# Optimization experiments

Measured on AMD Instinct MI355X. Metric: run time of the kernel, lower is better.

## Reference

```python
import jax, jax.numpy as jnp
import numpy as np

N = 100000
E = 1600000
D_IN = 128
HID = 128
OUT = 64


def _sage_conv(x, edge_index, W_l, W_r, b, num_nodes):
    # PyG SAGEConv (aggr='mean'): out = lin_l(mean_{j in N(i)} x_j) + lin_r(x_i)
    src, dst = edge_index[0], edge_index[1]
    msgs = x[src]  # [E, d] gather from source nodes
    summed = jax.ops.segment_sum(msgs, dst, num_segments=num_nodes)  # [N, d]
    cnt = jax.ops.segment_sum(jnp.ones((msgs.shape[0],), x.dtype), dst, num_segments=num_nodes)
    agg = summed / jnp.maximum(cnt, 1.0)[:, None]  # mean; isolated nodes -> 0
    return agg @ W_l + b + x @ W_r


def setup_inputs() -> dict:
    key = jax.random.key(0)
    ks = jax.random.split(key, 8)
    x = jax.random.normal(ks[0], (N, D_IN), dtype=jnp.float32)
    edge_index = jax.random.randint(ks[1], (2, E), 0, N, dtype=jnp.int64)
    s1 = 1.0 / np.sqrt(D_IN)
    s2 = 1.0 / np.sqrt(HID)
    W_l1 = jax.random.uniform(ks[2], (D_IN, HID), jnp.float32, -s1, s1)
    W_r1 = jax.random.uniform(ks[3], (D_IN, HID), jnp.float32, -s1, s1)
    b1 = jnp.zeros((HID,), jnp.float32)
    W_l2 = jax.random.uniform(ks[4], (HID, OUT), jnp.float32, -s2, s2)
    W_r2 = jax.random.uniform(ks[5], (HID, OUT), jnp.float32, -s2, s2)
    b2 = jnp.zeros((OUT,), jnp.float32)
    return {"x": x, "edge_index": edge_index, "W_l1": W_l1, "W_r1": W_r1,
            "b1": b1, "W_l2": W_l2, "W_r2": W_r2, "b2": b2}


def reference(x, edge_index, W_l1, W_r1, b1, W_l2, W_r2, b2):
    h = _sage_conv(x, edge_index, W_l1, W_r1, b1, N)
    h = jax.nn.relu(h)
    out = _sage_conv(h, edge_index, W_l2, W_r2, b2, N)
    return out
```

## Files before the change

kernel.cpp:

```cpp
#include <hip/hip_runtime.h>
#include <hip/hip_fp16.h>

typedef __attribute__((ext_vector_type(8))) short bf16x8;
typedef __attribute__((ext_vector_type(4))) float f32x4;

__device__ __forceinline__ f32x4 mfma16(bf16x8 a, bf16x8 b, f32x4 c) {
    return __builtin_amdgcn_mfma_f32_16x16x32_bf16(a, b, c, 0, 0, 0);
}

__device__ __forceinline__ unsigned short bf16_rte(float f) {
    unsigned int u = __float_as_uint(f);
    unsigned int r = (u + 0x7FFFu + ((u >> 16) & 1u)) >> 16;
    return (unsigned short)r;
}
__device__ __forceinline__ float bf16_f(unsigned short h) {
    return __uint_as_float(((unsigned int)h) << 16);
}

__device__ __forceinline__ void split8h(bf16x8 raw, bf16x8& hi, bf16x8& lo) {
#pragma unroll
    for (int j = 0; j < 8; ++j) {
        float f = __half2float(__ushort_as_half((unsigned short)raw[j]));
        unsigned short h = bf16_rte(f);
        hi[j] = (short)h;
        lo[j] = (short)bf16_rte(f - bf16_f(h));
    }
}

__device__ __forceinline__ void acc8(uint4 r, float4& A0, float4& A1) {
    float2 v0 = __half22float2(*(const __half2*)&r.x);
    float2 v1 = __half22float2(*(const __half2*)&r.y);
    float2 v2 = __half22float2(*(const __half2*)&r.z);
    float2 v3 = __half22float2(*(const __half2*)&r.w);
    A0.x += v0.x; A0.y += v0.y; A0.z += v1.x; A0.w += v1.y;
    A1.x += v2.x; A1.y += v2.y; A1.z += v3.x; A1.w += v3.y;
}

__device__ __forceinline__ void acc4(uint2 r, float4& A) {
    float2 v0 = __half22float2(*(const __half2*)&r.x);
    float2 v1 = __half22float2(*(const __half2*)&r.y);
    A.x += v0.x; A.y += v0.y; A.z += v1.x; A.w += v1.y;
}

#define MAXNB 1024

__global__ __launch_bounds__(256) void k_prep(
    const float* __restrict__ Wl1, const float* __restrict__ Wr1,
    const float* __restrict__ Wl2, const float* __restrict__ Wr2,
    unsigned short* __restrict__ w1ah, unsigned short* __restrict__ w1al,
    unsigned short* __restrict__ w1bh, unsigned short* __restrict__ w1bl,
    unsigned short* __restrict__ w2ah, unsigned short* __restrict__ w2al,
    unsigned short* __restrict__ w2bh, unsigned short* __restrict__ w2bl,
    const float* __restrict__ x, unsigned short* __restrict__ x16,
    const int* __restrict__ dst, int* __restrict__ bcnt,
    int E, int chunk, int xb, int nb, int total8) {
    __shared__ int hh[MAXNB];
    int b = blockIdx.x;
    int t = threadIdx.x;
    if (b < 192) {
        const float* W;
        unsigned short *hi, *lo;
        int F, e;
        if (b < 64)       { W = Wl1; hi = w1ah; lo = w1al; F = 128; e = b * 256 + t; }
        else if (b < 128) { W = Wr1; hi = w1bh; lo = w1bl; F = 128; e = (b - 64) * 256 + t; }
        else if (b < 160) { W = Wl2; hi = w2ah; lo = w2al; F = 64;  e = (b - 128) * 256 + t; }
        else              { W = Wr2; hi = w2bh; lo = w2bl; F = 64;  e = (b - 160) * 256 + t; }
        if (e >= 128 * F) return;
        int col = e >> 7, k = e & 127;
        float v = W[(size_t)k * F + col];
        unsigned short h = bf16_rte(v);
        hi[e] = h;
        lo[e] = bf16_rte(v - bf16_f(h));
    } else if (b < 192 + xb) {
        int i = (b - 192) * 256 + t;
        if (i >= total8) return;
        const float4* xp = (const float4*)x + (size_t)i * 2;
        float4 a = xp[0], bb = xp[1];
        bf16x8 o;
        o[0] = (short)__half_as_ushort(__float2half_rn(a.x));
        o[1] = (short)__half_as_ushort(__float2half_rn(a.y));
        o[2] = (short)__half_as_ushort(__float2half_rn(a.z));
        o[3] = (short)__half_as_ushort(__float2half_rn(a.w));
        o[4] = (short)__half_as_ushort(__float2half_rn(bb.x));
        o[5] = (short)__half_as_ushort(__float2half_rn(bb.y));
        o[6] = (short)__half_as_ushort(__float2half_rn(bb.z));
        o[7] = (short)__half_as_ushort(__float2half_rn(bb.w));
        *(bf16x8*)&x16[(size_t)i * 8] = o;
    } else {
        int cb = b - 192 - xb;
        for (int i = t; i < nb; i += 256) hh[i] = 0;
        __syncthreads();
        int base = cb * chunk;
        int end = min(base + chunk, E);
        for (int i = base + t; i < end; i += 256) atomicAdd(&hh[dst[i] >> 7], 1);
        __syncthreads();
        for (int i = t; i < nb; i += 256)
            if (hh[i]) atomicAdd(&bcnt[i], hh[i]);
    }
}


__global__ void k_bscan(const int* __restrict__ bcnt, int* __restrict__ boff,
                        int* __restrict__ bcur, int nb) {
    __shared__ int sh[1024];
    int t = threadIdx.x;
    int v = (t < nb) ? bcnt[t] : 0;
    sh[t] = v;
    __syncthreads();
    for (int off = 1; off < 1024; off <<= 1) {
        int u = (t >= off) ? sh[t - off] : 0;
        __syncthreads();
        sh[t] += u;
        __syncthreads();
    }
    if (t < nb) {
        int ex = sh[t] - v;
        boff[t] = ex;
        bcur[t] = ex;
    }
}

__global__ __launch_bounds__(256) void k_bscatter(
    const int* __restrict__ src, const int* __restrict__ dst,
    int* __restrict__ bcur, unsigned int* __restrict__ pairs,
    int E, int chunk, int nb) {
    __shared__ int h[MAXNB];
    __shared__ int curs[MAXNB];
    int t = threadIdx.x;
    for (int i = t; i < nb; i += 256) h[i] = 0;
    __syncthreads();
    int base = blockIdx.x * chunk;
    int end = min(base + chunk, E);
    for (int i = base + t; i < end; i += 256) atomicAdd(&h[dst[i] >> 7], 1);
    __syncthreads();
    for (int i = t; i < nb; i += 256)
        curs[i] = h[i] ? atomicAdd(&bcur[i], h[i]) : 0;
    __syncthreads();
    for (int i = base + t; i < end; i += 256) {
        int d = dst[i];
        int p = atomicAdd(&curs[d >> 7], 1);
        pairs[p] = ((unsigned int)(d & 127) << 25) | (unsigned int)src[i];
    }
}

__global__ __launch_bounds__(256) void k_build(
    const unsigned int* __restrict__ pairs, const int* __restrict__ boff,
    int* __restrict__ csr, int* __restrict__ start, int* __restrict__ deg,
    int n, int nb, int E) {
    __shared__ int scnt[128];
    __shared__ int soff[128];
    __shared__ int cur[128];
    int b = blockIdx.x;
    int t = threadIdx.x;
    int base = boff[b];
    int end = (b + 1 < nb) ? boff[b + 1] : E;
    if (t < 128) scnt[t] = 0;
    __syncthreads();
    for (int i = base + t; i < end; i += 256) {
        unsigned int e = pairs[i];
        atomicAdd(&scnt[e >> 25], 1);
    }
    __syncthreads();
    if (t < 128) soff[t] = scnt[t];
    __syncthreads();
    for (int off = 1; off < 128; off <<= 1) {
        int val = 0;
        if (t < 128 && t >= off) val = soff[t - off];
        __syncthreads();
        if (t < 128) soff[t] += val;
        __syncthreads();
    }
    if (t < 128) {
        int c = scnt[t];
        int ex = soff[t] - c;
        int node = b * 128 + t;
        if (node < n) {
            start[node] = base + ex;
            deg[node] = c;
        }
        cur[t] = base + ex;
    }
    __syncthreads();
    for (int i = base + t; i < end; i += 256) {
        unsigned int e = pairs[i];
        int p = atomicAdd(&cur[e >> 25], 1);
        csr[p] = (int)(e & 0x1FFFFFFu);
    }
}

#define SR 40

__global__ __launch_bounds__(256) void aggF(
    const unsigned short* __restrict__ tab, const int* __restrict__ csr,
    const int* __restrict__ start, const int* __restrict__ deg,
    unsigned short* __restrict__ outm, int n) {
    int gid = blockIdx.x * blockDim.x + threadIdx.x;
    int wave = gid >> 6, lane = gid & 63;
    int sub = lane >> 4, fl = lane & 15;
    int node = wave * 4 + sub;
    if (node >= n) return;
    int s = start[node], d = deg[node];
    float4 A0 = {0.f, 0.f, 0.f, 0.f}, A1 = {0.f, 0.f, 0.f, 0.f};
    int j = 0;
    if (d >= 4) {
        int i0 = csr[s], i1 = csr[s + 1], i2 = csr[s + 2], i3 = csr[s + 3];
        for (; j + 8 <= d; j += 4) {
            int n0 = csr[s + j + 4], n1 = csr[s + j + 5];
            int n2 = csr[s + j + 6], n3 = csr[s + j + 7];
            uint4 r0 = ((const uint4*)(tab + (size_t)i0 * 128))[fl];
            uint4 r1 = ((const uint4*)(tab + (size_t)i1 * 128))[fl];
            uint4 r2 = ((const uint4*)(tab + (size_t)i2 * 128))[fl];
            uint4 r3 = ((const uint4*)(tab + (size_t)i3 * 128))[fl];
            acc8(r0, A0, A1); acc8(r1, A0, A1);
            acc8(r2, A0, A1); acc8(r3, A0, A1);
            i0 = n0; i1 = n1; i2 = n2; i3 = n3;
        }
        {
            uint4 r0 = ((const uint4*)(tab + (size_t)i0 * 128))[fl];
            uint4 r1 = ((const uint4*)(tab + (size_t)i1 * 128))[fl];
            uint4 r2 = ((const uint4*)(tab + (size_t)i2 * 128))[fl];
            uint4 r3 = ((const uint4*)(tab + (size_t)i3 * 128))[fl];
            acc8(r0, A0, A1); acc8(r1, A0, A1);
            acc8(r2, A0, A1); acc8(r3, A0, A1);
            j += 4;
        }
    }
    for (; j < d; ++j)
        acc8(((const uint4*)(tab + (size_t)csr[s + j] * 128))[fl], A0, A1);
    float inv = 1.0f / (float)max(d, 1);
    __half2 h0 = __floats2half2_rn(A0.x * inv, A0.y * inv);
    __half2 h1 = __floats2half2_rn(A0.z * inv, A0.w * inv);
    __half2 h2 = __floats2half2_rn(A1.x * inv, A1.y * inv);
    __half2 h3 = __floats2half2_rn(A1.z * inv, A1.w * inv);
    uint4 w;
    w.x = *(unsigned int*)&h0;
    w.y = *(unsigned int*)&h1;
    w.z = *(unsigned int*)&h2;
    w.w = *(unsigned int*)&h3;
    *(uint4*)&outm[(size_t)node * 128 + fl * 8] = w;
}

__global__ __launch_bounds__(256, 4) void fused12(
    const unsigned short* __restrict__ X, const unsigned short* __restrict__ XM,
    const unsigned short* __restrict__ W0H, const unsigned short* __restrict__ W0L,
    const unsigned short* __restrict__ W1H, const unsigned short* __restrict__ W1L,
    const float* __restrict__ b1,
    const unsigned short* __restrict__ W2aH, const unsigned short* __restrict__ W2aL,
    const unsigned short* __restrict__ W2bH, const unsigned short* __restrict__ W2bL,
    const float* __restrict__ b2,
    unsigned short* __restrict__ p16, float* __restrict__ outF, int n) {
    constexpr int CT = 2;
    __shared__ unsigned short lds[4 * 64 * SR];
    unsigned short* hi0 = lds;
    unsigned short* hi1 = lds + 64 * SR;
    unsigned short* lo0 = lds + 2 * 64 * SR;
    unsigned short* lo1 = lds + 3 * 64 * SR;

    int t = threadIdx.x;
    int wv = t >> 6, l = t & 63, q = l >> 4, nl = l & 15;
    int node0 = blockIdx.x * 64;
    int sn = t >> 2, q4 = t & 3;
    int gn = min(node0 + sn, n - 1);
    int sbase = sn * SR + q4 * 8;

    bf16x8 xr[4], s1r[4];
    {
        const unsigned short* p = X + (size_t)gn * 128 + q4 * 8;
#pragma unroll
        for (int c = 0; c < 4; ++c) xr[c] = *(const bf16x8*)(p + c * 32);
        const unsigned short* pm = XM + (size_t)gn * 128 + q4 * 8;
#pragma unroll
        for (int c = 0; c < 4; ++c) s1r[c] = *(const bf16x8*)(pm + c * 32);
    }

    f32x4 acc[4][CT];
#pragma unroll
    for (int a = 0; a < 4; ++a)
#pragma unroll
        for (int b = 0; b < CT; ++b) acc[a][b] = (f32x4){0.f, 0.f, 0.f, 0.f};

    bf16x8 whA[CT], wlA[CT], whB[CT], wlB[CT];
    int wcX = wv * 32;

#define LOAD_W(AH, AL, WHp, WLp, CC)                                       \
    {                                                                      \
        _Pragma("unroll") for (int uu = 0; uu < CT; ++uu) {                \
            int wb = (wcX + uu * 16 + nl) * 128 + (CC) * 32 + q * 8;       \
            AH[uu] = *(const bf16x8*)&(WHp)[wb];                           \
            AL[uu] = *(const bf16x8*)&(WLp)[wb];                           \
        }                                                                  \
    }

#define STAGE_CHUNK(HP, LP, RAW)                                           \
    {                                                                      \
        bf16x8 _hi, _lo;                                                   \
        split8h(RAW, _hi, _lo);                                            \
        *(bf16x8*)&(HP)[sbase] = _hi;                                      \
        *(bf16x8*)&(LP)[sbase] = _lo;                                      \
    }

#define MFMA_CHUNK(HP, LP, WHR, WLR)                                       \
    {                                                                      \
        bf16x8 ah[4], al[4];                                               \
        _Pragma("unroll") for (int tt = 0; tt < 4; ++tt) {                 \
            int off = (tt * 16 + nl) * SR + q * 8;                         \
            ah[tt] = *(const bf16x8*)&(HP)[off];                           \
            al[tt] = *(const bf16x8*)&(LP)[off];                           \
        }                                                                  \
        _Pragma("unroll") for (int tt = 0; tt < 4; ++tt)                   \
            _Pragma("unroll") for (int uu = 0; uu < CT; ++uu) {            \
                f32x4 a = acc[tt][uu];                                     \
                a = mfma16(al[tt], WHR[uu], a);                            \
                a = mfma16(ah[tt], WLR[uu], a);                            \
                a = mfma16(ah[tt], WHR[uu], a);                            \
                acc[tt][uu] = a;                                           \
            }                                                              \
    }

#define PHASE(RSRC, WHp, WLp)                                              \
    LOAD_W(whA, wlA, WHp, WLp, 0);                                         \
    STAGE_CHUNK(hi0, lo0, RSRC[0]);                                        \
    __syncthreads();                                                       \
    LOAD_W(whB, wlB, WHp, WLp, 1);                                         \
    STAGE_CHUNK(hi1, lo1, RSRC[1]);                                        \
    MFMA_CHUNK(hi0, lo0, whA, wlA);                                        \
    __syncthreads();                                                       \
    LOAD_W(whA, wlA, WHp, WLp, 2);                                         \
    STAGE_CHUNK(hi0, lo0, RSRC[2]);                                        \
    MFMA_CHUNK(hi1, lo1, whB, wlB);                                        \
    __syncthreads();                                                       \
    LOAD_W(whB, wlB, WHp, WLp, 3);                                         \
    STAGE_CHUNK(hi1, lo1, RSRC[3]);                                        \
    MFMA_CHUNK(hi0, lo0, whA, wlA);                                        \
    __syncthreads();                                                       \
    MFMA_CHUNK(hi1, lo1, whB, wlB);                                        \
    __syncthreads();

    PHASE(xr, W0H, W0L);
    PHASE(s1r, W1H, W1L);

    unsigned short* tb = lds;
#pragma unroll
    for (int uu = 0; uu < CT; ++uu) {
        int col = wcX + uu * 16 + nl;
        float bv = b1[col];
#pragma unroll
        for (int tt = 0; tt < 4; ++tt)
#pragma unroll
            for (int r = 0; r < 4; ++r) {
                float vv = fmaxf(acc[tt][uu][r] + bv, 0.f);
                tb[(tt * 16 + q * 4 + r) * 136 + col] =
                    __half_as_ushort(__float2half_rn(vv));
            }
    }
    __syncthreads();
    bf16x8 hreg[4];
    {
        const unsigned short* sp = tb + sn * 136 + q4 * 8;
#pragma unroll
        for (int c = 0; c < 4; ++c) hreg[c] = *(const bf16x8*)(sp + c * 32);
    }
    __syncthreads();

#pragma unroll
    for (int a = 0; a < 4; ++a)
#pragma unroll
        for (int b = 0; b < CT; ++b) acc[a][b] = (f32x4){0.f, 0.f, 0.f, 0.f};
    int ysel = wv >> 1;
    wcX = (wv & 1) * 32;
    const unsigned short* W2H = ysel ? W2bH : W2aH;
    const unsigned short* W2L = ysel ? W2bL : W2aL;
    PHASE(hreg, W2H, W2L);

#undef PHASE
#undef MFMA_CHUNK
#undef STAGE_CHUNK
#undef LOAD_W

    if (ysel) {
#pragma unroll
        for (int uu = 0; uu < CT; ++uu) {
            int col = wcX + uu * 16 + nl;
            float bv = b2[col];
#pragma unroll
            for (int tt = 0; tt < 4; ++tt)
#pragma unroll
                for (int r = 0; r < 4; ++r) {
                    int node = node0 + tt * 16 + q * 4 + r;
                    if (node < n) outF[(size_t)node * 64 + col] = acc[tt][uu][r] + bv;
                }
        }
    } else {
        unsigned short* tbu = lds;
#pragma unroll
        for (int uu = 0; uu < CT; ++uu) {
            int col = wcX + uu * 16 + nl;
#pragma unroll
            for (int tt = 0; tt < 4; ++tt)
#pragma unroll
                for (int r = 0; r < 4; ++r)
                    tbu[(tt * 16 + q * 4 + r) * 72 + col] =
                        __half_as_ushort(__float2half_rn(acc[tt][uu][r]));
        }
    }
    __syncthreads();
    {
        int node = node0 + sn;
        if (node < n) {
            const unsigned short* spu = lds + sn * 72 + q4 * 16;
            unsigned short* dpu = p16 + (size_t)node * 64 + q4 * 16;
            *(bf16x8*)dpu = *(const bf16x8*)spu;
            *(bf16x8*)(dpu + 8) = *(const bf16x8*)(spu + 8);
        }
    }
}

__global__ __launch_bounds__(256) void aggP(
    const unsigned short* __restrict__ tab, const int* __restrict__ csr,
    const int* __restrict__ start, const int* __restrict__ deg,
    float* __restrict__ outF, int n) {
    int gid = blockIdx.x * blockDim.x + threadIdx.x;
    int wave = gid >> 6, lane = gid & 63;
    int sub = lane >> 4, fl = lane & 15;
    int node = wave * 4 + sub;
    if (node >= n) return;
    int s = start[node], d = deg[node];
    float4 A = {0.f, 0.f, 0.f, 0.f};
    int j = 0;
    if (d >= 8) {
        int idx[8];
#pragma unroll
        for (int k = 0; k < 8; ++k) idx[k] = csr[s + k];
        for (; j + 16 <= d; j += 8) {
            uint2 rr[8];
#pragma unroll
            for (int k = 0; k < 8; ++k)
                rr[k] = ((const uint2*)(tab + (size_t)idx[k] * 64))[fl];
#pragma unroll
            for (int k = 0; k < 8; ++k) idx[k] = csr[s + j + 8 + k];
#pragma unroll
            for (int k = 0; k < 8; ++k) acc4(rr[k], A);
        }
        {
            uint2 rr[8];
#pragma unroll
            for (int k = 0; k < 8; ++k)
                rr[k] = ((const uint2*)(tab + (size_t)idx[k] * 64))[fl];
#pragma unroll
            for (int k = 0; k < 8; ++k) acc4(rr[k], A);
            j += 8;
        }
    }
    for (; j < d; ++j)
        acc4(((const uint2*)(tab + (size_t)csr[s + j] * 64))[fl], A);
    float inv = 1.0f / (float)max(d, 1);
    float* op = outF + (size_t)node * 64 + fl * 4;
    float4 cur = *(float4*)op;
    cur.x += A.x * inv;
    cur.y += A.y * inv;
    cur.z += A.z * inv;
    cur.w += A.w * inv;
    *(float4*)op = cur;
}


extern "C" void kernel_launch(void* const* d_in, const int* in_sizes, int n_in,
                              void* d_out, int out_size, void* d_ws, size_t ws_size,
                              hipStream_t stream) {
    const float* x   = (const float*)d_in[0];
    const int*   ei  = (const int*)d_in[1];
    const float* Wl1 = (const float*)d_in[2];
    const float* Wr1 = (const float*)d_in[3];
    const float* b1  = (const float*)d_in[4];
    const float* Wl2 = (const float*)d_in[5];
    const float* Wr2 = (const float*)d_in[6];
    const float* b2  = (const float*)d_in[7];
    float* out = (float*)d_out;

    int Nn = in_sizes[0] / 128;
    int E  = in_sizes[1] / 2;
    const int* src = ei;
    const int* dst = ei + E;
    int nb = (Nn + 127) / 128;

    char* ws = (char*)d_ws;
    auto alloc = [&](size_t bytes) -> char* {
        char* pp = ws;
        ws += (bytes + 255) / 256 * 256;
        return pp;
    };
    int* bcnt   = (int*)alloc((size_t)nb * 4);
    int* boff   = (int*)alloc((size_t)nb * 4);
    int* bcur   = (int*)alloc((size_t)nb * 4);
    int* start  = (int*)alloc((size_t)Nn * 4);
    int* deg    = (int*)alloc((size_t)Nn * 4);
    int* csr    = (int*)alloc((size_t)E * 4);
    unsigned short* x16  = (unsigned short*)alloc((size_t)Nn * 128 * 2);
    unsigned short* xm16 = (unsigned short*)alloc((size_t)Nn * 128 * 2);
    unsigned short* p16  = (unsigned short*)alloc((size_t)Nn * 64 * 2);
    unsigned short* w1ah = (unsigned short*)alloc(128 * 128 * 2);
    unsigned short* w1al = (unsigned short*)alloc(128 * 128 * 2);
    unsigned short* w1bh = (unsigned short*)alloc(128 * 128 * 2);
    unsigned short* w1bl = (unsigned short*)alloc(128 * 128 * 2);
    unsigned short* w2ah = (unsigned short*)alloc(64 * 128 * 2);
    unsigned short* w2al = (unsigned short*)alloc(64 * 128 * 2);
    unsigned short* w2bh = (unsigned short*)alloc(64 * 128 * 2);
    unsigned short* w2bl = (unsigned short*)alloc(64 * 128 * 2);
    unsigned int* pairs = (unsigned int*)p16;

    hipMemsetAsync(bcnt, 0, (size_t)nb * 4, stream);

    int total8 = Nn * 16;
    int xb = (total8 + 255) / 256;
    int nchunks = 256;
    int chunk = (E + nchunks - 1) / nchunks;
    k_prep<<<192 + xb + nchunks, 256, 0, stream>>>(
        Wl1, Wr1, Wl2, Wr2,
        w1ah, w1al, w1bh, w1bl, w2ah, w2al, w2bh, w2bl,
        x, x16, dst, bcnt, E, chunk, xb, nb, total8);

    k_bscan<<<1, 1024, 0, stream>>>(bcnt, boff, bcur, nb);
    k_bscatter<<<nchunks, 256, 0, stream>>>(src, dst, bcur, pairs, E, chunk, nb);
    k_build<<<nb, 256, 0, stream>>>(pairs, boff, csr, start, deg, Nn, nb, E);

    int gb = (Nn + 63) / 64;
    int ga = (Nn + 15) / 16;
    aggF<<<ga, 256, 0, stream>>>(x16, csr, start, deg, xm16, Nn);
    fused12<<<gb, 256, 0, stream>>>(x16, xm16,
                                    w1bh, w1bl, w1ah, w1al, b1,
                                    w2ah, w2al, w2bh, w2bl, b2,
                                    p16, out, Nn);
    aggP<<<ga, 256, 0, stream>>>(p16, csr, start, deg, out, Nn);
}
```

Before: 329.2 us.

## Build CSR with per-node global atomics instead of two-level bucket sort

Replaces the bucketed counting sort (block-level LDS histograms, pair scatter into buckets, then per-bucket local sort) with per-node degree counting via global atomics, a two-level scan for node offsets, and a direct atomic scatter of sources into CSR. This removes the intermediate packed-pairs pass and the k_build kernel, reducing edge-array traffic. In exchange it relies on millions of global atomics to scattered addresses and adds extra small launches; neighbor order within a row becomes nondeterministic.

```diff
diff --git a/kernel.cpp b/kernel.cpp
--- a/kernel.cpp
+++ b/kernel.cpp
@@ -52,9 +52,8 @@
     unsigned short* __restrict__ w2ah, unsigned short* __restrict__ w2al,
     unsigned short* __restrict__ w2bh, unsigned short* __restrict__ w2bl,
     const float* __restrict__ x, unsigned short* __restrict__ x16,
-    const int* __restrict__ dst, int* __restrict__ bcnt,
-    int E, int chunk, int xb, int nb, int total8) {
-    __shared__ int hh[MAXNB];
+    const int* __restrict__ dst, int* __restrict__ deg,
+    int E, int chunk, int xb, int total8) {
     int b = blockIdx.x;
     int t = threadIdx.x;
     if (b < 192) {
@@ -88,20 +87,30 @@
         *(bf16x8*)&x16[(size_t)i * 8] = o;
     } else {
         int cb = b - 192 - xb;
-        for (int i = t; i < nb; i += 256) hh[i] = 0;
-        __syncthreads();
         int base = cb * chunk;
         int end = min(base + chunk, E);
-        for (int i = base + t; i < end; i += 256) atomicAdd(&hh[dst[i] >> 7], 1);
+        for (int i = base + t; i < end; i += 256)
+            atomicAdd(&deg[dst[i]], 1);
+    }
+}
+
+
+__global__ __launch_bounds__(128) void k_bsum(
+    const int* __restrict__ deg, int* __restrict__ bcnt, int n) {
+    __shared__ int sh[128];
+    int b = blockIdx.x, t = threadIdx.x;
+    int node = b * 128 + t;
+    sh[t] = (node < n) ? deg[node] : 0;
+    __syncthreads();
+    for (int off = 64; off > 0; off >>= 1) {
+        if (t < off) sh[t] += sh[t + off];
         __syncthreads();
-        for (int i = t; i < nb; i += 256)
-            if (hh[i]) atomicAdd(&bcnt[i], hh[i]);
-    }
-}
-
+    }
+    if (t == 0) bcnt[b] = sh[0];
+}
 
 __global__ void k_bscan(const int* __restrict__ bcnt, int* __restrict__ boff,
-                        int* __restrict__ bcur, int nb) {
+                        int nb) {
     __shared__ int sh[1024];
     int t = threadIdx.x;
     int v = (t < nb) ? bcnt[t] : 0;
@@ -113,78 +122,41 @@
         sh[t] += u;
         __syncthreads();
     }
-    if (t < nb) {
-        int ex = sh[t] - v;
-        boff[t] = ex;
-        bcur[t] = ex;
-    }
-}
-
-__global__ __launch_bounds__(256) void k_bscatter(
+    if (t < nb) boff[t] = sh[t] - v;
+}
+
+__global__ __launch_bounds__(128) void k_nscan(
+    const int* __restrict__ deg, const int* __restrict__ boff,
+    int* __restrict__ start, int* __restrict__ cur, int n) {
+    __shared__ int sh[128];
+    int b = blockIdx.x, t = threadIdx.x;
+    int node = b * 128 + t;
+    int v = (node < n) ? deg[node] : 0;
+    sh[t] = v;
+    __syncthreads();
+    for (int off = 1; off < 128; off <<= 1) {
+        int u = (t >= off) ? sh[t - off] : 0;
+        __syncthreads();
+        sh[t] += u;
+        __syncthreads();
+    }
+    if (node < n) {
+        int ex = sh[t] - v + boff[b];
+        start[node] = ex;
+        cur[node] = ex;
+    }
+}
+
+__global__ __launch_bounds__(256) void k_scatter(
     const int* __restrict__ src, const int* __restrict__ dst,
-    int* __restrict__ bcur, unsigned int* __restrict__ pairs,
-    int E, int chunk, int nb) {
-    __shared__ int h[MAXNB];
-    __shared__ int curs[MAXNB];
-    int t = threadIdx.x;
-    for (int i = t; i < nb; i += 256) h[i] = 0;
-    __syncthreads();
-    int base = blockIdx.x * chunk;
-    int end = min(base + chunk, E);
-    for (int i = base + t; i < end; i += 256) atomicAdd(&h[dst[i] >> 7], 1);
-    __syncthreads();
-    for (int i = t; i < nb; i += 256)
-        curs[i] = h[i] ? atomicAdd(&bcur[i], h[i]) : 0;
-    __syncthreads();
-    for (int i = base + t; i < end; i += 256) {
+    int* __restrict__ cur, int* __restrict__ csr, int E) {
+    int i0 = blockIdx.x * 256 + threadIdx.x;
+    int stride = gridDim.x * 256;
+    for (int i = i0; i < E; i += stride) {
         int d = dst[i];
-        int p = atomicAdd(&curs[d >> 7], 1);
-        pairs[p] = ((unsigned int)(d & 127) << 25) | (unsigned int)src[i];
-    }
-}
-
-__global__ __launch_bounds__(256) void k_build(
-    const unsigned int* __restrict__ pairs, const int* __restrict__ boff,
-    int* __restrict__ csr, int* __restrict__ start, int* __restrict__ deg,
-    int n, int nb, int E) {
-    __shared__ int scnt[128];
-    __shared__ int soff[128];
-    __shared__ int cur[128];
-    int b = blockIdx.x;
-    int t = threadIdx.x;
-    int base = boff[b];
-    int end = (b + 1 < nb) ? boff[b + 1] : E;
-    if (t < 128) scnt[t] = 0;
-    __syncthreads();
-    for (int i = base + t; i < end; i += 256) {
-        unsigned int e = pairs[i];
-        atomicAdd(&scnt[e >> 25], 1);
-    }
-    __syncthreads();
-    if (t < 128) soff[t] = scnt[t];
-    __syncthreads();
-    for (int off = 1; off < 128; off <<= 1) {
-        int val = 0;
-        if (t < 128 && t >= off) val = soff[t - off];
-        __syncthreads();
-        if (t < 128) soff[t] += val;
-        __syncthreads();
-    }
-    if (t < 128) {
-        int c = scnt[t];
-        int ex = soff[t] - c;
-        int node = b * 128 + t;
-        if (node < n) {
-            start[node] = base + ex;
-            deg[node] = c;
-        }
-        cur[t] = base + ex;
-    }
-    __syncthreads();
-    for (int i = base + t; i < end; i += 256) {
-        unsigned int e = pairs[i];
-        int p = atomicAdd(&cur[e >> 25], 1);
-        csr[p] = (int)(e & 0x1FFFFFFu);
+        int s = src[i];
+        int p = atomicAdd(&cur[d], 1);
+        csr[p] = s;
     }
 }
 
@@ -491,7 +463,7 @@
     };
     int* bcnt   = (int*)alloc((size_t)nb * 4);
     int* boff   = (int*)alloc((size_t)nb * 4);
-    int* bcur   = (int*)alloc((size_t)nb * 4);
+    int* cur    = (int*)alloc((size_t)Nn * 4);
     int* start  = (int*)alloc((size_t)Nn * 4);
     int* deg    = (int*)alloc((size_t)Nn * 4);
     int* csr    = (int*)alloc((size_t)E * 4);
@@ -506,9 +478,8 @@
     unsigned short* w2al = (unsigned short*)alloc(64 * 128 * 2);
     unsigned short* w2bh = (unsigned short*)alloc(64 * 128 * 2);
     unsigned short* w2bl = (unsigned short*)alloc(64 * 128 * 2);
-    unsigned int* pairs = (unsigned int*)p16;
-
-    hipMemsetAsync(bcnt, 0, (size_t)nb * 4, stream);
+
+    hipMemsetAsync(deg, 0, (size_t)Nn * 4, stream);
 
     int total8 = Nn * 16;
     int xb = (total8 + 255) / 256;
@@ -517,11 +488,12 @@
     k_prep<<<192 + xb + nchunks, 256, 0, stream>>>(
         Wl1, Wr1, Wl2, Wr2,
         w1ah, w1al, w1bh, w1bl, w2ah, w2al, w2bh, w2bl,
-        x, x16, dst, bcnt, E, chunk, xb, nb, total8);
-
-    k_bscan<<<1, 1024, 0, stream>>>(bcnt, boff, bcur, nb);
-    k_bscatter<<<nchunks, 256, 0, stream>>>(src, dst, bcur, pairs, E, chunk, nb);
-    k_build<<<nb, 256, 0, stream>>>(pairs, boff, csr, start, deg, Nn, nb, E);
+        x, x16, dst, deg, E, chunk, xb, total8);
+
+    k_bsum<<<nb, 128, 0, stream>>>(deg, bcnt, Nn);
+    k_bscan<<<1, 1024, 0, stream>>>(bcnt, boff, nb);
+    k_nscan<<<nb, 128, 0, stream>>>(deg, boff, start, cur, Nn);
+    k_scatter<<<2048, 256, 0, stream>>>(src, dst, cur, csr, E);
 
     int gb = (Nn + 63) / 64;
     int ga = (Nn + 15) / 16;
```

Measured after the change: 477.0 us. +44.9%, slower.
